# Performance work log

Measured on AMD Instinct MI355X. Metric: run time of the kernel, lower is better.

## Reference

```python
import jax, jax.numpy as jnp
import numpy as np

N = 512      # state dim n
K = 8        # num_regimes
H = 256      # hidden dim for g0/g1/gate MLPs
B = 8192     # batch
INIT_SCALE = 0.1


def _mlp(x, w1, b1, w2, b2, w3, b3):
    # 2 hidden SiLU layers + linear head (matches ScalarMLP/GateNet with num_layers=2)
    h = jax.nn.silu(x @ w1 + b1)
    h = jax.nn.silu(h @ w2 + b2)
    return h @ w3 + b3


def setup_inputs() -> dict:
    key = jax.random.key(0)
    ks = jax.random.split(key, 12)

    def lin(k, fi, fo):
        kw, kb = jax.random.split(k)
        s = 1.0 / np.sqrt(fi)  # torch nn.Linear default init range
        w = jax.random.uniform(kw, (fi, fo), minval=-s, maxval=s, dtype=jnp.float32)
        b = jax.random.uniform(kb, (fo,), minval=-s, maxval=s, dtype=jnp.float32)
        return w, b

    g0_w1, g0_b1 = lin(ks[0], N, H)
    g0_w2, g0_b2 = lin(ks[1], H, H)
    g0_w3, g0_b3 = lin(ks[2], H, 1)
    g1_w1, g1_b1 = lin(ks[3], N, H)
    g1_w2, g1_b2 = lin(ks[4], H, H)
    g1_w3, g1_b3 = lin(ks[5], H, 1)
    gt_w1, gt_b1 = lin(ks[6], N, H)
    gt_w2, gt_b2 = lin(ks[7], H, H)
    gt_w3, gt_b3 = lin(ks[8], H, K)
    W = jax.random.uniform(ks[9], (K, N, N), minval=-INIT_SCALE, maxval=INIT_SCALE, dtype=jnp.float32)
    z = jax.random.normal(ks[10], (B, 2 * N), dtype=jnp.float32)
    return dict(z=z,
                g0_w1=g0_w1, g0_b1=g0_b1, g0_w2=g0_w2, g0_b2=g0_b2, g0_w3=g0_w3, g0_b3=g0_b3,
                g1_w1=g1_w1, g1_b1=g1_b1, g1_w2=g1_w2, g1_b2=g1_b2, g1_w3=g1_w3, g1_b3=g1_b3,
                gt_w1=gt_w1, gt_b1=gt_b1, gt_w2=gt_w2, gt_b2=gt_b2, gt_w3=gt_w3, gt_b3=gt_b3,
                W=W)


def reference(z,
              g0_w1, g0_b1, g0_w2, g0_b2, g0_w3, g0_b3,
              g1_w1, g1_b1, g1_w2, g1_b2, g1_w3, g1_b3,
              gt_w1, gt_b1, gt_w2, gt_b2, gt_w3, gt_b3,
              W):
    n = W.shape[-1]
    x0, x1 = z[:, :n], z[:, n:]

    def U(x0_, x1_):
        e0 = jnp.sum(_mlp(x0_, g0_w1, g0_b1, g0_w2, g0_b2, g0_w3, g0_b3))  # scalar
        e1 = jnp.sum(_mlp(x1_, g1_w1, g1_b1, g1_w2, g1_b2, g1_w3, g1_b3))
        alpha = jax.nn.softmax(_mlp(x0_, gt_w1, gt_b1, gt_w2, gt_b2, gt_w3, gt_b3), axis=-1)  # [B,K]
        # per-sample per-regime bilinear x1^T W_k x0 -> avoids materializing [B,n,n] W_eff
        q = jnp.einsum('bi,kij,bj->bk', x1_, W, x0_)
        return e0 + e1 + jnp.sum(alpha * q)

    grad_x0, grad_x1 = jax.grad(U, argnums=(0, 1))(x0, x1)
    return jnp.concatenate([-grad_x0, -grad_x1], axis=-1)  # [B, 2n]
```

## Files before the change

### kernel.cpp

```cpp
#include <hip/hip_runtime.h>
#include <cstdint>
#include <cstddef>

constexpr int BTOT = 8192, N = 512, H = 256, K = 8;

typedef __attribute__((ext_vector_type(8))) short short8v;
typedef __attribute__((ext_vector_type(4))) float f32x4;

__device__ __forceinline__ float bf2f(unsigned short u) {
    return __uint_as_float(((uint32_t)u) << 16);
}
__device__ __forceinline__ unsigned short f2bf(float f) {
    uint32_t u = __float_as_uint(f);
    uint32_t r = (u + 0x7FFFu + ((u >> 16) & 1u)) >> 16;
    return (unsigned short)r;
}

typedef __attribute__((address_space(3))) unsigned int lds_uint;
typedef __attribute__((address_space(1))) const unsigned int glob_uint;
__device__ __forceinline__ void async16(const unsigned short* g, unsigned short* l) {
    __builtin_amdgcn_global_load_lds((glob_uint*)g, (lds_uint*)l, 16, 0, 0);
}

struct GArg {
    const unsigned short* A;
    const unsigned short* Bt;
    const float* bias;
    const unsigned short* dmul;
    unsigned short* ob;
    unsigned short* ob2;
    float* of;
    int lda, ldbt, Ka, lddm, ldob, ldof;
};

enum { EPI_BF = 0, EPI_FWD = 1, EPI_BWD2 = 2, EPI_NEG = 3, EPI_NEGW = 4 };

template<int EPI>
__global__ __launch_bounds__(256) void gemm_g(GArg ga0, GArg ga1, GArg ga2)
{
    const int z = blockIdx.z;
    const GArg g = (z == 0) ? ga0 : (z == 1) ? ga1 : ga2;

    __shared__ __attribute__((aligned(16))) unsigned short As[128 * 32];
    __shared__ __attribute__((aligned(16))) unsigned short Bs[128 * 32];
    const int tid = threadIdx.x;
    const int lane = tid & 63, wave = tid >> 6;
    const int m0 = blockIdx.y * 128, n0 = blockIdx.x * 128;
    const int wr = (wave >> 1) * 64, wc = (wave & 1) * 64;
    const int rr = lane & 15, kb = (lane >> 4) * 8;

    const int r0 = tid >> 2, ko0 = (tid & 3) << 3;
    const unsigned short* gA0 = g.A + (size_t)(m0 + r0) * g.lda + ko0;
    const unsigned short* gA1 = g.A + (size_t)(m0 + r0 + 64) * g.lda + ko0;
    const unsigned short* gB0 = g.Bt + (size_t)(n0 + r0) * g.ldbt + ko0;
    const unsigned short* gB1 = g.Bt + (size_t)(n0 + r0 + 64) * g.ldbt + ko0;
    unsigned short* lA0 = As + tid * 8;
    unsigned short* lA1 = As + (tid + 256) * 8;
    unsigned short* lB0 = Bs + tid * 8;
    unsigned short* lB1 = Bs + (tid + 256) * 8;

    f32x4 acc[4][4];
    #pragma unroll
    for (int i = 0; i < 4; ++i)
        #pragma unroll
        for (int j = 0; j < 4; ++j) acc[i][j] = (f32x4){0.f, 0.f, 0.f, 0.f};

    for (int k0 = 0; k0 < g.Ka; k0 += 32) {
        async16(gA0 + k0, lA0);
        async16(gA1 + k0, lA1);
        async16(gB0 + k0, lB0);
        async16(gB1 + k0, lB1);
        __syncthreads();

        short8v af[4], bfr[4];
        #pragma unroll
        for (int i = 0; i < 4; ++i)
            af[i] = *(const short8v*)(As + (wr + i * 16 + rr) * 32 + kb);
        #pragma unroll
        for (int j = 0; j < 4; ++j)
            bfr[j] = *(const short8v*)(Bs + (wc + j * 16 + rr) * 32 + kb);
        #pragma unroll
        for (int i = 0; i < 4; ++i)
            #pragma unroll
            for (int j = 0; j < 4; ++j)
                acc[i][j] = __builtin_amdgcn_mfma_f32_16x16x32_bf16(af[i], bfr[j], acc[i][j], 0, 0, 0);
        __syncthreads();
    }

    const int orow = (lane >> 4) * 4;
    #pragma unroll
    for (int i = 0; i < 4; ++i) {
        #pragma unroll
        for (int e = 0; e < 4; ++e) {
            const int row = m0 + wr + i * 16 + orow + e;
            #pragma unroll
            for (int j = 0; j < 4; ++j) {
                const int col = n0 + wc + rr + j * 16;
                float v = acc[i][j][e];
                if constexpr (EPI == EPI_BF) {
                    g.ob[(size_t)row * g.ldob + col] = f2bf(v);
                } else if constexpr (EPI == EPI_FWD) {
                    float p = v + g.bias[col];
                    float s = 1.f / (1.f + expf(-p));
                    if (g.ob) g.ob[(size_t)row * g.ldob + col] = f2bf(p * s);
                    g.ob2[(size_t)row * g.ldob + col] = f2bf(s * (1.f + p * (1.f - s)));
                } else if constexpr (EPI == EPI_BWD2) {
                    float t = v * bf2f(g.dmul[(size_t)row * g.lddm + col]);
                    g.ob[(size_t)row * g.ldob + col] = f2bf(t);
                } else if constexpr (EPI == EPI_NEG) {
                    g.of[(size_t)row * g.ldof + col] -= v;
                } else {
                    g.of[(size_t)row * g.ldof + col] = -v;
                }
            }
        }
    }
}

__global__ __launch_bounds__(256) void k_cvt_z(const float* __restrict__ z,
                                               unsigned short* __restrict__ o) {
    int g = (blockIdx.x * 256 + threadIdx.x) * 4;
    float4 v = *(const float4*)(z + g);
    ushort4 u;
    u.x = f2bf(v.x); u.y = f2bf(v.y); u.z = f2bf(v.z); u.w = f2bf(v.w);
    *(ushort4*)(o + g) = u;
}

__global__ __launch_bounds__(256) void k_transpose_w(const float* __restrict__ W,
    unsigned short* __restrict__ Wbf, unsigned short* __restrict__ WTbf)
{
    __shared__ float t[32][33];
    int k = blockIdx.z;
    int i0 = blockIdx.y * 32, j0 = blockIdx.x * 32;
    int tj = threadIdx.x & 31, ti = threadIdx.x >> 5;
    const float* Wk = W + (size_t)k * N * N;
    #pragma unroll
    for (int r = 0; r < 32; r += 8) {
        float v = Wk[(size_t)(i0 + ti + r) * N + j0 + tj];
        t[ti + r][tj] = v;
        Wbf[(size_t)k * N * N + (size_t)(i0 + ti + r) * N + j0 + tj] = f2bf(v);
    }
    __syncthreads();
    #pragma unroll
    for (int r = 0; r < 32; r += 8)
        WTbf[(size_t)k * N * N + (size_t)(j0 + ti + r) * N + i0 + tj] = f2bf(t[tj][ti + r]);
}

struct CvtJob { const float* src; unsigned short* dst; int ls, ld, cols32, tiles, trans; };
struct CvtTable { CvtJob j[12]; };

__global__ __launch_bounds__(256) void k_cvt_w(CvtTable T)
{
    int t = blockIdx.x;
    int ji = 0;
    while (t >= T.j[ji].tiles) { t -= T.j[ji].tiles; ++ji; }
    CvtJob jb = T.j[ji];
    int i0 = (t / jb.cols32) * 32, c0 = (t % jb.cols32) * 32;
    int tc = threadIdx.x & 31, tr = threadIdx.x >> 5;
    if (!jb.trans) {
        #pragma unroll
        for (int r = 0; r < 32; r += 8)
            jb.dst[(size_t)(i0 + tr + r) * jb.ld + c0 + tc] =
                f2bf(jb.src[(size_t)(i0 + tr + r) * jb.ls + c0 + tc]);
    } else {
        __shared__ float tt[32][33];
        #pragma unroll
        for (int r = 0; r < 32; r += 8)
            tt[tr + r][tc] = jb.src[(size_t)(i0 + tr + r) * jb.ls + c0 + tc];
        __syncthreads();
        #pragma unroll
        for (int r = 0; r < 32; r += 8)
            jb.dst[(size_t)(c0 + tr + r) * jb.ld + i0 + tc] = f2bf(tt[tc][tr + r]);
    }
}

__global__ __launch_bounds__(256) void k_head_s(const unsigned short* __restrict__ h2t,
    const float* __restrict__ w3t, const float* __restrict__ b3t,
    float* __restrict__ s)
{
    int t = threadIdx.x;
    int bl = t >> 3, k = t & 7;
    int b = blockIdx.x * 32 + bl;
    const unsigned short* ar = h2t + (size_t)b * H;
    float acc = b3t[k];
    for (int h = 0; h < H; ++h) acc += bf2f(ar[h]) * w3t[h * K + k];
    s[b * K + k] = acc;
}

__global__ __launch_bounds__(256) void k_q(const unsigned short* __restrict__ v0,
    const float* __restrict__ zc, float* __restrict__ q)
{
    int w = threadIdx.x >> 6, lane = threadIdx.x & 63;
    int idx = blockIdx.x * 4 + w;
    int b = idx >> 3, k = idx & 7;
    const unsigned short* vr = v0 + ((size_t)b * K + k) * N;
    const float* xr = zc + (size_t)b * 1024 + 512;
    short8v vv = *(const short8v*)(vr + lane * 8);
    float s = 0.f;
    #pragma unroll
    for (int t = 0; t < 8; ++t) s += bf2f((unsigned short)vv[t]) * xr[lane * 8 + t];
    for (int off = 32; off; off >>= 1) s += __shfl_down(s, off, 64);
    if (lane == 0) q[idx] = s;
}

__global__ __launch_bounds__(256) void k_d(const float* __restrict__ s,
    const float* __restrict__ q, float* __restrict__ alpha,
    float* __restrict__ dd, int Bc)
{
    int b = blockIdx.x * 256 + threadIdx.x;
    if (b >= Bc) return;
    float sv[K], qv[K];
    float m = -1e30f;
    #pragma unroll
    for (int k = 0; k < K; ++k) { sv[k] = s[b * K + k]; m = fmaxf(m, sv[k]); }
    float sum = 0.f;
    #pragma unroll
    for (int k = 0; k < K; ++k) { sv[k] = expf(sv[k] - m); sum += sv[k]; }
    float inv = 1.f / sum, qbar = 0.f;
    #pragma unroll
    for (int k = 0; k < K; ++k) { sv[k] *= inv; qv[k] = q[b * K + k]; qbar += sv[k] * qv[k]; }
    #pragma unroll
    for (int k = 0; k < K; ++k) {
        alpha[b * K + k] = sv[k];
        dd[b * K + k] = sv[k] * (qv[k] - qbar);
    }
}

__global__ __launch_bounds__(256) void k_u2(
    const unsigned short* __restrict__ d2_0, const unsigned short* __restrict__ d2_1,
    const unsigned short* __restrict__ d2_t,
    const float* __restrict__ w3_0, const float* __restrict__ w3_1,
    const float* __restrict__ w3t, const float* __restrict__ dd,
    unsigned short* __restrict__ u2_0, unsigned short* __restrict__ u2_1,
    unsigned short* __restrict__ u2_t)
{
    int g = blockIdx.x * 256 + threadIdx.x;
    int h = g & (H - 1), b = g >> 8;
    u2_0[g] = f2bf(w3_0[h] * bf2f(d2_0[g]));
    u2_1[g] = f2bf(w3_1[h] * bf2f(d2_1[g]));
    float s = 0.f;
    #pragma unroll
    for (int k = 0; k < K; ++k) s += w3t[h * K + k] * dd[b * K + k];
    u2_t[g] = f2bf(s * bf2f(d2_t[g]));
}

__global__ __launch_bounds__(256) void k_gxq2(const unsigned short* __restrict__ v0,
    const unsigned short* __restrict__ v1, const float* __restrict__ alpha,
    float* __restrict__ out)
{
    int g = blockIdx.x * 256 + threadIdx.x;
    int b = g >> 6, jb = (g & 63) << 3;
    float al[K];
    #pragma unroll
    for (int k = 0; k < K; ++k) al[k] = alpha[b * K + k];
    const unsigned short* pv0 = v0 + (size_t)b * K * N + jb;
    const unsigned short* pv1 = v1 + (size_t)b * K * N + jb;
    float s0[8] = {}, s1[8] = {};
    #pragma unroll
    for (int k = 0; k < K; ++k) {
        short8v w1 = *(const short8v*)(pv1 + (size_t)k * N);
        short8v w0 = *(const short8v*)(pv0 + (size_t)k * N);
        #pragma unroll
        for (int t = 0; t < 8; ++t) {
            s0[t] += al[k] * bf2f((unsigned short)w1[t]);
            s1[t] += al[k] * bf2f((unsigned short)w0[t]);
        }
    }
    float* o0 = out + (size_t)b * 1024 + jb;
    float* o1 = o0 + 512;
    float4 x0 = *(float4*)o0, x1 = *(float4*)(o0 + 4);
    x0.x -= s0[0]; x0.y -= s0[1]; x0.z -= s0[2]; x0.w -= s0[3];
    x1.x -= s0[4]; x1.y -= s0[5]; x1.z -= s0[6]; x1.w -= s0[7];
    *(float4*)o0 = x0; *(float4*)(o0 + 4) = x1;
    float4 y0 = *(float4*)o1, y1 = *(float4*)(o1 + 4);
    y0.x -= s1[0]; y0.y -= s1[1]; y0.z -= s1[2]; y0.w -= s1[3];
    y1.x -= s1[4]; y1.y -= s1[5]; y1.z -= s1[6]; y1.w -= s1[7];
    *(float4*)o1 = y0; *(float4*)(o1 + 4) = y1;
}

extern "C" void kernel_launch(void* const* d_in, const int* in_sizes, int n_in,
                              void* d_out, int out_size, void* d_ws, size_t ws_size,
                              hipStream_t stream) {
    const float* z     = (const float*)d_in[0];
    const float* g0_w1 = (const float*)d_in[1];  const float* g0_b1 = (const float*)d_in[2];
    const float* g0_w2 = (const float*)d_in[3];  const float* g0_b2 = (const float*)d_in[4];
    const float* g0_w3 = (const float*)d_in[5];
    const float* g1_w1 = (const float*)d_in[7];  const float* g1_b1 = (const float*)d_in[8];
    const float* g1_w2 = (const float*)d_in[9];  const float* g1_b2 = (const float*)d_in[10];
    const float* g1_w3 = (const float*)d_in[11];
    const float* gt_w1 = (const float*)d_in[13]; const float* gt_b1 = (const float*)d_in[14];
    const float* gt_w2 = (const float*)d_in[15]; const float* gt_b2 = (const float*)d_in[16];
    const float* gt_w3 = (const float*)d_in[17]; const float* gt_b3 = (const float*)d_in[18];
    const float* W     = (const float*)d_in[19];
    float* out = (float*)d_out;

    char* wsb = (char*)d_ws;
    size_t off = 0;
    auto aus = [&](size_t n) -> unsigned short* {
        unsigned short* r = (unsigned short*)(wsb + off);
        off += ((n * 2 + 255) & ~(size_t)255);
        return r;
    };
    auto af4 = [&](size_t n) -> float* {
        float* r = (float*)(wsb + off);
        off += ((n * 4 + 255) & ~(size_t)255);
        return r;
    };

    unsigned short* Zbf  = aus((size_t)BTOT * 1024);
    unsigned short* Wbf  = aus((size_t)K * N * N);
    unsigned short* WTbf = aus((size_t)K * N * N);
    unsigned short* w1T[3], *w2T[3], *w2N[3];
    for (int i = 0; i < 3; ++i) w1T[i] = aus((size_t)H * N);
    for (int i = 0; i < 3; ++i) w2T[i] = aus((size_t)H * H);
    for (int i = 0; i < 3; ++i) w2N[i] = aus((size_t)H * H);
    unsigned short* w1N1  = aus((size_t)N * H);
    unsigned short* w1cat = aus((size_t)N * 2 * H);
    unsigned short* h1[3], *d1b[3], *d2b[3], *u2[3];
    for (int i = 0; i < 3; ++i) h1[i]  = aus((size_t)BTOT * H);
    for (int i = 0; i < 3; ++i) d1b[i] = aus((size_t)BTOT * H);
    for (int i = 0; i < 3; ++i) d2b[i] = aus((size_t)BTOT * H);
    for (int i = 0; i < 3; ++i) u2[i]  = aus((size_t)BTOT * H);
    unsigned short* h2t   = aus((size_t)BTOT * H);
    unsigned short* t2cat = aus((size_t)BTOT * 512);
    unsigned short* t21   = aus((size_t)BTOT * H);
    float* sbuf = af4((size_t)BTOT * K);
    float* qbuf = af4((size_t)BTOT * K);
    float* abuf = af4((size_t)BTOT * K);
    float* dbuf = af4((size_t)BTOT * K);

    int Bcv = BTOT;
    while (off + 2 * (((size_t)Bcv * K * N * 2 + 255) & ~(size_t)255) > ws_size && Bcv > 128)
        Bcv >>= 1;
    unsigned short* v0 = aus((size_t)Bcv * K * N);
    unsigned short* v1 = aus((size_t)Bcv * K * N);
    const bool full = (Bcv == BTOT);

    const dim3 blk(256);

    if (!full)
        hipMemsetAsync(d_out, 0, (size_t)out_size * sizeof(float), stream);

    k_cvt_z<<<BTOT * 1024 / (256 * 4), blk, 0, stream>>>(z, Zbf);
    k_transpose_w<<<dim3(N / 32, N / 32, K), blk, 0, stream>>>(W, Wbf, WTbf);

    CvtTable T;
    int nj = 0, tot = 0;
    auto addjob = [&](const float* src, int ls, unsigned short* dst, int ld,
                      int rows, int cols, int trans) {
        CvtJob jb; jb.src = src; jb.dst = dst; jb.ls = ls; jb.ld = ld;
        jb.cols32 = cols / 32; jb.tiles = (rows / 32) * (cols / 32); jb.trans = trans;
        T.j[nj++] = jb; tot += jb.tiles;
    };
    addjob(g0_w1, H, w1T[0], N, N, H, 1);
    addjob(g1_w1, H, w1T[1], N, N, H, 1);
    addjob(gt_w1, H, w1T[2], N, N, H, 1);
    addjob(g0_w2, H, w2T[0], H, H, H, 1);
    addjob(g1_w2, H, w2T[1], H, H, H, 1);
    addjob(gt_w2, H, w2T[2], H, H, H, 1);
    addjob(g0_w2, H, w2N[0], H, H, H, 0);
    addjob(g1_w2, H, w2N[1], H, H, H, 0);
    addjob(gt_w2, H, w2N[2], H, H, H, 0);
    addjob(g1_w1, H, w1N1, H, N, H, 0);
    addjob(g0_w1, H, w1cat, 2 * H, N, H, 0);
    addjob(gt_w1, H, w1cat + H, 2 * H, N, H, 0);
    k_cvt_w<<<tot, blk, 0, stream>>>(T);

    auto mk = [](const unsigned short* A, int lda, const unsigned short* Bt, int ldbt, int Ka) {
        GArg g; g.A = A; g.Bt = Bt; g.bias = nullptr; g.dmul = nullptr;
        g.ob = nullptr; g.ob2 = nullptr; g.of = nullptr;
        g.lda = lda; g.ldbt = ldbt; g.Ka = Ka; g.lddm = 0; g.ldob = 0; g.ldof = 0;
        return g;
    };

    {
        const float* bs[3] = {g0_b1, g1_b1, gt_b1};
        GArg a[3];
        for (int i = 0; i < 3; ++i) {
            a[i] = mk(Zbf + (i == 1 ? 512 : 0), 1024, w1T[i], N, N);
            a[i].bias = bs[i]; a[i].ob = h1[i]; a[i].ob2 = d1b[i]; a[i].ldob = H;
        }
        gemm_g<EPI_FWD><<<dim3(H / 128, BTOT / 128, 3), blk, 0, stream>>>(a[0], a[1], a[2]);
    }
    {
        const float* bs[3] = {g0_b2, g1_b2, gt_b2};
        GArg a[3];
        for (int i = 0; i < 3; ++i) {
            a[i] = mk(h1[i], H, w2T[i], H, H);
            a[i].bias = bs[i]; a[i].ob = (i == 2) ? h2t : nullptr;
            a[i].ob2 = d2b[i]; a[i].ldob = H;
        }
        gemm_g<EPI_FWD><<<dim3(H / 128, BTOT / 128, 3), blk, 0, stream>>>(a[0], a[1], a[2]);
    }
    k_head_s<<<BTOT / 32, blk, 0, stream>>>(h2t, gt_w3, gt_b3, sbuf);

    for (int cb = 0; cb < BTOT; cb += Bcv) {
        GArg a[2];
        a[0] = mk(Zbf + (size_t)cb * 1024, 1024, Wbf, N, N);
        a[0].ob = v0; a[0].ldob = K * N;
        a[1] = mk(Zbf + (size_t)cb * 1024 + 512, 1024, WTbf, N, N);
        a[1].ob = v1; a[1].ldob = K * N;
        gemm_g<EPI_BF><<<dim3(K * N / 128, Bcv / 128, 2), blk, 0, stream>>>(a[0], a[1], a[1]);

        k_q<<<Bcv * K / 4, blk, 0, stream>>>(v0, z + (size_t)cb * 1024, qbuf + (size_t)cb * K);
        k_d<<<(Bcv + 255) / 256, blk, 0, stream>>>(sbuf + (size_t)cb * K, qbuf + (size_t)cb * K,
                                                   abuf + (size_t)cb * K, dbuf + (size_t)cb * K, Bcv);
        if (!full)
            k_gxq2<<<Bcv * 64 / 256, blk, 0, stream>>>(v0, v1, abuf + (size_t)cb * K,
                                                       out + (size_t)cb * 1024);
    }

    k_u2<<<BTOT * H / 256, blk, 0, stream>>>(d2b[0], d2b[1], d2b[2],
                                             g0_w3, g1_w3, gt_w3, dbuf,
                                             u2[0], u2[1], u2[2]);

    {
        GArg a[3];
        a[0] = mk(u2[0], H, w2N[0], H, H);
        a[0].dmul = d1b[0]; a[0].lddm = H; a[0].ob = t2cat;     a[0].ldob = 512;
        a[1] = mk(u2[1], H, w2N[1], H, H);
        a[1].dmul = d1b[1]; a[1].lddm = H; a[1].ob = t21;       a[1].ldob = H;
        a[2] = mk(u2[2], H, w2N[2], H, H);
        a[2].dmul = d1b[2]; a[2].lddm = H; a[2].ob = t2cat + H; a[2].ldob = 512;
        gemm_g<EPI_BWD2><<<dim3(H / 128, BTOT / 128, 3), blk, 0, stream>>>(a[0], a[1], a[2]);
    }
    {
        GArg a[2];
        a[0] = mk(t2cat, 512, w1cat, 2 * H, 512);
        a[0].of = out;       a[0].ldof = 1024;
        a[1] = mk(t21, H, w1N1, H, H);
        a[1].of = out + 512; a[1].ldof = 1024;
        if (full)
            gemm_g<EPI_NEGW><<<dim3(N / 128, BTOT / 128, 2), blk, 0, stream>>>(a[0], a[1], a[1]);
        else
            gemm_g<EPI_NEG><<<dim3(N / 128, BTOT / 128, 2), blk, 0, stream>>>(a[0], a[1], a[1]);
    }

    if (full)
        k_gxq2<<<BTOT * 64 / 256, blk, 0, stream>>>(v0, v1, abuf, out);
}
```

Before: 276.2 us.

## Double-buffer GEMM LDS with swizzle, fuse gxq into final GEMM epilogue

The GEMM mainloop now double-buffers LDS tiles so the next K-slice loads while MFMAs run, and it XOR-swizzles the LDS layout to reduce bank conflicts. The final gradient GEMM gains an epilogue that subtracts the alpha-weighted v0/v1 term directly, which replaces the separate k_gxq2 pass and its read-modify-write of the output. k_head_s vectorises its row loads, and k_q reads the bf16 copy of z instead of fp32. The cost is twice the LDS per block, which may lower occupancy, and k_q now reads x1 in bf16 rather than fp32, which slightly lowers precision.

```diff
diff --git a/kernel.cpp b/kernel.cpp
--- a/kernel.cpp
+++ b/kernel.cpp
@@ -27,13 +27,15 @@
     const unsigned short* Bt;
     const float* bias;
     const unsigned short* dmul;
+    const float* alpha;
+    const unsigned short* vsub;
     unsigned short* ob;
     unsigned short* ob2;
     float* of;
     int lda, ldbt, Ka, lddm, ldob, ldof;
 };
 
-enum { EPI_BF = 0, EPI_FWD = 1, EPI_BWD2 = 2, EPI_NEG = 3, EPI_NEGW = 4 };
+enum { EPI_BF = 0, EPI_FWD = 1, EPI_BWD2 = 2, EPI_NEG = 3, EPI_NEGV = 4 };
 
 template<int EPI>
 __global__ __launch_bounds__(256) void gemm_g(GArg ga0, GArg ga1, GArg ga2)
@@ -41,23 +43,21 @@
     const int z = blockIdx.z;
     const GArg g = (z == 0) ? ga0 : (z == 1) ? ga1 : ga2;
 
-    __shared__ __attribute__((aligned(16))) unsigned short As[128 * 32];
-    __shared__ __attribute__((aligned(16))) unsigned short Bs[128 * 32];
+    __shared__ __attribute__((aligned(16))) unsigned short As[2][128 * 32];
+    __shared__ __attribute__((aligned(16))) unsigned short Bs[2][128 * 32];
     const int tid = threadIdx.x;
     const int lane = tid & 63, wave = tid >> 6;
     const int m0 = blockIdx.y * 128, n0 = blockIdx.x * 128;
     const int wr = (wave >> 1) * 64, wc = (wave & 1) * 64;
-    const int rr = lane & 15, kb = (lane >> 4) * 8;
-
-    const int r0 = tid >> 2, ko0 = (tid & 3) << 3;
+    const int rr = lane & 15;
+    const int kb = ((lane >> 4) ^ (lane & 3)) << 3;
+
+    const int r0 = tid >> 2;
+    const int ko0 = (((tid & 3) ^ (r0 & 3)) << 3);
     const unsigned short* gA0 = g.A + (size_t)(m0 + r0) * g.lda + ko0;
     const unsigned short* gA1 = g.A + (size_t)(m0 + r0 + 64) * g.lda + ko0;
     const unsigned short* gB0 = g.Bt + (size_t)(n0 + r0) * g.ldbt + ko0;
     const unsigned short* gB1 = g.Bt + (size_t)(n0 + r0 + 64) * g.ldbt + ko0;
-    unsigned short* lA0 = As + tid * 8;
-    unsigned short* lA1 = As + (tid + 256) * 8;
-    unsigned short* lB0 = Bs + tid * 8;
-    unsigned short* lB1 = Bs + (tid + 256) * 8;
 
     f32x4 acc[4][4];
     #pragma unroll
@@ -65,26 +65,39 @@
         #pragma unroll
         for (int j = 0; j < 4; ++j) acc[i][j] = (f32x4){0.f, 0.f, 0.f, 0.f};
 
-    for (int k0 = 0; k0 < g.Ka; k0 += 32) {
-        async16(gA0 + k0, lA0);
-        async16(gA1 + k0, lA1);
-        async16(gB0 + k0, lB0);
-        async16(gB1 + k0, lB1);
-        __syncthreads();
-
+    const int nt = g.Ka >> 5;
+
+    async16(gA0, &As[0][tid * 8]);
+    async16(gA1, &As[0][(tid + 256) * 8]);
+    async16(gB0, &Bs[0][tid * 8]);
+    async16(gB1, &Bs[0][(tid + 256) * 8]);
+    asm volatile("s_waitcnt vmcnt(0)" ::: "memory");
+    __builtin_amdgcn_s_barrier();
+
+    int cur = 0;
+    for (int t = 0; t < nt; ++t) {
+        if (t + 1 < nt) {
+            const int k0 = (t + 1) << 5;
+            async16(gA0 + k0, &As[cur ^ 1][tid * 8]);
+            async16(gA1 + k0, &As[cur ^ 1][(tid + 256) * 8]);
+            async16(gB0 + k0, &Bs[cur ^ 1][tid * 8]);
+            async16(gB1 + k0, &Bs[cur ^ 1][(tid + 256) * 8]);
+        }
         short8v af[4], bfr[4];
         #pragma unroll
         for (int i = 0; i < 4; ++i)
-            af[i] = *(const short8v*)(As + (wr + i * 16 + rr) * 32 + kb);
+            af[i] = *(const short8v*)(&As[cur][(wr + i * 16 + rr) * 32 + kb]);
         #pragma unroll
         for (int j = 0; j < 4; ++j)
-            bfr[j] = *(const short8v*)(Bs + (wc + j * 16 + rr) * 32 + kb);
+            bfr[j] = *(const short8v*)(&Bs[cur][(wc + j * 16 + rr) * 32 + kb]);
         #pragma unroll
         for (int i = 0; i < 4; ++i)
             #pragma unroll
             for (int j = 0; j < 4; ++j)
                 acc[i][j] = __builtin_amdgcn_mfma_f32_16x16x32_bf16(af[i], bfr[j], acc[i][j], 0, 0, 0);
-        __syncthreads();
+        asm volatile("s_waitcnt vmcnt(0)" ::: "memory");
+        __builtin_amdgcn_s_barrier();
+        cur ^= 1;
     }
 
     const int orow = (lane >> 4) * 4;
@@ -93,24 +106,37 @@
         #pragma unroll
         for (int e = 0; e < 4; ++e) {
             const int row = m0 + wr + i * 16 + orow + e;
-            #pragma unroll
-            for (int j = 0; j < 4; ++j) {
-                const int col = n0 + wc + rr + j * 16;
-                float v = acc[i][j][e];
-                if constexpr (EPI == EPI_BF) {
-                    g.ob[(size_t)row * g.ldob + col] = f2bf(v);
-                } else if constexpr (EPI == EPI_FWD) {
-                    float p = v + g.bias[col];
-                    float s = 1.f / (1.f + expf(-p));
-                    if (g.ob) g.ob[(size_t)row * g.ldob + col] = f2bf(p * s);
-                    g.ob2[(size_t)row * g.ldob + col] = f2bf(s * (1.f + p * (1.f - s)));
-                } else if constexpr (EPI == EPI_BWD2) {
-                    float t = v * bf2f(g.dmul[(size_t)row * g.lddm + col]);
-                    g.ob[(size_t)row * g.ldob + col] = f2bf(t);
-                } else if constexpr (EPI == EPI_NEG) {
-                    g.of[(size_t)row * g.ldof + col] -= v;
-                } else {
-                    g.of[(size_t)row * g.ldof + col] = -v;
+            if constexpr (EPI == EPI_NEGV) {
+                float al[K];
+                #pragma unroll
+                for (int kk = 0; kk < K; ++kk) al[kk] = g.alpha[(size_t)row * K + kk];
+                #pragma unroll
+                for (int j = 0; j < 4; ++j) {
+                    const int col = n0 + wc + rr + j * 16;
+                    const unsigned short* vp = g.vsub + (size_t)row * (K * N) + col;
+                    float sub = 0.f;
+                    #pragma unroll
+                    for (int kk = 0; kk < K; ++kk) sub += al[kk] * bf2f(vp[(size_t)kk * N]);
+                    g.of[(size_t)row * g.ldof + col] = -acc[i][j][e] - sub;
+                }
+            } else {
+                #pragma unroll
+                for (int j = 0; j < 4; ++j) {
+                    const int col = n0 + wc + rr + j * 16;
+                    float v = acc[i][j][e];
+                    if constexpr (EPI == EPI_BF) {
+                        g.ob[(size_t)row * g.ldob + col] = f2bf(v);
+                    } else if constexpr (EPI == EPI_FWD) {
+                        float p = v + g.bias[col];
+                        float s = 1.f / (1.f + expf(-p));
+                        if (g.ob) g.ob[(size_t)row * g.ldob + col] = f2bf(p * s);
+                        g.ob2[(size_t)row * g.ldob + col] = f2bf(s * (1.f + p * (1.f - s)));
+                    } else if constexpr (EPI == EPI_BWD2) {
+                        float t = v * bf2f(g.dmul[(size_t)row * g.lddm + col]);
+                        g.ob[(size_t)row * g.ldob + col] = f2bf(t);
+                    } else if constexpr (EPI == EPI_NEG) {
+                        g.of[(size_t)row * g.ldof + col] -= v;
+                    }
                 }
             }
         }
@@ -183,22 +209,29 @@
     int b = blockIdx.x * 32 + bl;
     const unsigned short* ar = h2t + (size_t)b * H;
     float acc = b3t[k];
-    for (int h = 0; h < H; ++h) acc += bf2f(ar[h]) * w3t[h * K + k];
+    for (int h0 = 0; h0 < H; h0 += 8) {
+        short8v hv = *(const short8v*)(ar + h0);
+        #pragma unroll
+        for (int u = 0; u < 8; ++u)
+            acc += bf2f((unsigned short)hv[u]) * w3t[(h0 + u) * K + k];
+    }
     s[b * K + k] = acc;
 }
 
 __global__ __launch_bounds__(256) void k_q(const unsigned short* __restrict__ v0,
-    const float* __restrict__ zc, float* __restrict__ q)
+    const unsigned short* __restrict__ zb, float* __restrict__ q)
 {
     int w = threadIdx.x >> 6, lane = threadIdx.x & 63;
     int idx = blockIdx.x * 4 + w;
     int b = idx >> 3, k = idx & 7;
     const unsigned short* vr = v0 + ((size_t)b * K + k) * N;
-    const float* xr = zc + (size_t)b * 1024 + 512;
+    const unsigned short* xr = zb + (size_t)b * 1024 + 512;
     short8v vv = *(const short8v*)(vr + lane * 8);
+    short8v xv = *(const short8v*)(xr + lane * 8);
     float s = 0.f;
     #pragma unroll
-    for (int t = 0; t < 8; ++t) s += bf2f((unsigned short)vv[t]) * xr[lane * 8 + t];
+    for (int t = 0; t < 8; ++t)
+        s += bf2f((unsigned short)vv[t]) * bf2f((unsigned short)xv[t]);
     for (int off = 32; off; off >>= 1) s += __shfl_down(s, off, 64);
     if (lane == 0) q[idx] = s;
 }
@@ -368,6 +401,7 @@
 
     auto mk = [](const unsigned short* A, int lda, const unsigned short* Bt, int ldbt, int Ka) {
         GArg g; g.A = A; g.Bt = Bt; g.bias = nullptr; g.dmul = nullptr;
+        g.alpha = nullptr; g.vsub = nullptr;
         g.ob = nullptr; g.ob2 = nullptr; g.of = nullptr;
         g.lda = lda; g.ldbt = ldbt; g.Ka = Ka; g.lddm = 0; g.ldob = 0; g.ldof = 0;
         return g;
@@ -402,7 +436,7 @@
         a[1].ob = v1; a[1].ldob = K * N;
         gemm_g<EPI_BF><<<dim3(K * N / 128, Bcv / 128, 2), blk, 0, stream>>>(a[0], a[1], a[1]);
 
-        k_q<<<Bcv * K / 4, blk, 0, stream>>>(v0, z + (size_t)cb * 1024, qbuf + (size_t)cb * K);
+        k_q<<<Bcv * K / 4, blk, 0, stream>>>(v0, Zbf + (size_t)cb * 1024, qbuf + (size_t)cb * K);
         k_d<<<(Bcv + 255) / 256, blk, 0, stream>>>(sbuf + (size_t)cb * K, qbuf + (size_t)cb * K,
                                                    abuf + (size_t)cb * K, dbuf + (size_t)cb * K, Bcv);
         if (!full)
@@ -430,12 +464,12 @@
         a[0].of = out;       a[0].ldof = 1024;
         a[1] = mk(t21, H, w1N1, H, H);
         a[1].of = out + 512; a[1].ldof = 1024;
-        if (full)
-            gemm_g<EPI_NEGW><<<dim3(N / 128, BTOT / 128, 2), blk, 0, stream>>>(a[0], a[1], a[1]);
-        else
+        if (full) {
+            a[0].alpha = abuf; a[0].vsub = v1;
+            a[1].alpha = abuf; a[1].vsub = v0;
+            gemm_g<EPI_NEGV><<<dim3(N / 128, BTOT / 128, 2), blk, 0, stream>>>(a[0], a[1], a[1]);
+        } else {
             gemm_g<EPI_NEG><<<dim3(N / 128, BTOT / 128, 2), blk, 0, stream>>>(a[0], a[1], a[1]);
-    }
-
-    if (full)
-        k_gxq2<<<BTOT * 64 / 256, blk, 0, stream>>>(v0, v1, abuf, out);
-}
+        }
+    }
+}
```

Result: faster. 247.4 us (-10.4%).
